# Optimization experiments

Measured on AMD Instinct MI355X. Metric: run time of the kernel, lower is better.

## Reference

```python
import jax, jax.numpy as jnp
import numpy as np

IN_F = 2048
OUT_F = 8192
NUM_BLOCKS = 2097152  # (IN_F*OUT_F)//8
K = 4096
BLOCK = 8

def setup_inputs() -> dict:
    key = jax.random.key(0)
    k1, k2, k3, k4 = jax.random.split(key, 4)
    x = jax.random.normal(k1, (4, 2048, IN_F), dtype=jnp.float32)
    codebook = jax.random.normal(k2, (K, BLOCK), dtype=jnp.float32)
    indices = jax.random.randint(k3, (NUM_BLOCKS,), 0, K, dtype=jnp.int64)
    bias = jax.random.normal(k4, (OUT_F,), dtype=jnp.float32)
    return {"x": x, "codebook": codebook, "indices": indices, "bias": bias}

def reference(x, codebook, indices, bias):
    # Dequantize: gather codewords and reassemble the full weight matrix.
    # codebook[indices]: (num_blocks, block) -> flatten -> (in_f, out_f)
    W = codebook[indices].reshape(IN_F, OUT_F)
    # GPT-2 Conv1D: out = x @ W + b  (W is (in, out), not transposed)
    out = jnp.matmul(x, W) + bias
    return out
```

## Files before the change

### kernel.cpp

```cpp
#include <hip/hip_runtime.h>
#include <hip/hip_bf16.h>

typedef unsigned short ushort_t;
typedef __attribute__((ext_vector_type(8))) short short8;
typedef __attribute__((ext_vector_type(4))) float f32x4;

#define M_DIM 8192
#define N_DIM 8192
#define K_DIM 2048
#define BM 256
#define BN 256
#define BK 64
#define NT (K_DIM / BK)

__device__ __forceinline__ ushort_t f2bf(float f) {
    union { float f; unsigned u; } v; v.f = f;
    unsigned r = v.u + 0x7fffu + ((v.u >> 16) & 1u);
    return (ushort_t)(r >> 16);
}

__device__ __forceinline__ void async_copy16(const void* g, void* l) {
    __builtin_amdgcn_global_load_lds(
        (const __attribute__((address_space(1))) void*)g,
        (__attribute__((address_space(3))) void*)l, 16, 0, 0);
}

#define BAR() __builtin_amdgcn_s_barrier()
#define LGKM0() do { asm volatile("s_waitcnt lgkmcnt(0)" ::: "memory"); \
                     __builtin_amdgcn_sched_barrier(0); } while (0)

__global__ __launch_bounds__(256) void convert_x(const float* __restrict__ x,
                                                 ushort_t* __restrict__ A) {
    int t = blockIdx.x * 256 + threadIdx.x;
    const float4* p = (const float4*)x + (size_t)t * 2;
    float4 a = p[0], b = p[1];
    short8 o;
    o[0] = (short)f2bf(a.x); o[1] = (short)f2bf(a.y);
    o[2] = (short)f2bf(a.z); o[3] = (short)f2bf(a.w);
    o[4] = (short)f2bf(b.x); o[5] = (short)f2bf(b.y);
    o[6] = (short)f2bf(b.z); o[7] = (short)f2bf(b.w);
    *(short8*)(A + (size_t)t * 8) = o;
}

__global__ __launch_bounds__(256) void dequant_wt(const int* __restrict__ indices,
                                                  const float* __restrict__ codebook,
                                                  ushort_t* __restrict__ Bt) {
    int g = blockIdx.x;
    int i = blockIdx.y * 256 + threadIdx.x;
    int idx = indices[(size_t)i * 1024 + g];
    const float4* cb = (const float4*)(codebook + (size_t)idx * 8);
    float4 lo = cb[0], hi = cb[1];
    size_t base = (size_t)g * 8 * K_DIM + i;
    Bt[base + 0 * K_DIM] = f2bf(lo.x);
    Bt[base + 1 * K_DIM] = f2bf(lo.y);
    Bt[base + 2 * K_DIM] = f2bf(lo.z);
    Bt[base + 3 * K_DIM] = f2bf(lo.w);
    Bt[base + 4 * K_DIM] = f2bf(hi.x);
    Bt[base + 5 * K_DIM] = f2bf(hi.y);
    Bt[base + 6 * K_DIM] = f2bf(hi.z);
    Bt[base + 7 * K_DIM] = f2bf(hi.w);
}

__device__ __forceinline__ void load_af4(const ushort_t* p, const int (&off)[4][2],
                                         short8 (&fr)[4][2]) {
#pragma unroll
    for (int i = 0; i < 4; ++i)
#pragma unroll
        for (int kk = 0; kk < 2; ++kk)
            fr[i][kk] = *(const short8*)((const char*)p + off[i][kk]);
}

__device__ __forceinline__ void load_bf2(const ushort_t* p, const int (&off)[2][2],
                                         short8 (&fr)[2][2]) {
#pragma unroll
    for (int j = 0; j < 2; ++j)
#pragma unroll
        for (int kk = 0; kk < 2; ++kk)
            fr[j][kk] = *(const short8*)((const char*)p + off[j][kk]);
}

__device__ __forceinline__ void mfma16(const short8 (&af)[4][2], const short8 (&bf)[2][2],
                                       f32x4 (&acc)[8][4], int I0, int J0) {
    __builtin_amdgcn_s_setprio(1);
#pragma unroll
    for (int kk = 0; kk < 2; ++kk)
#pragma unroll
        for (int i = 0; i < 4; ++i)
#pragma unroll
            for (int j = 0; j < 2; ++j)
                acc[I0 + i][J0 + j] = __builtin_amdgcn_mfma_f32_16x16x32_bf16(
                    af[i][kk], bf[j][kk], acc[I0 + i][J0 + j], 0, 0, 0);
    __builtin_amdgcn_s_setprio(0);
}

__global__ __launch_bounds__(512, 2) void gemm_256_8phase(const ushort_t* __restrict__ A,
                                                          const ushort_t* __restrict__ Bt,
                                                          const float* __restrict__ bias,
                                                          float* __restrict__ C) {
    __shared__ __align__(16) ushort_t lds_a[2][2][128 * 64];
    __shared__ __align__(16) ushort_t lds_b[2][2][128 * 64];

    const int bid = blockIdx.x;
    const int x = bid & 7;
    const int q = bid >> 3;
    const int mt = ((x >> 1) << 2) + (q & 3) + (((q >> 5) & 1) << 4);
    const int nt = ((x & 1) << 3) + ((q >> 2) & 7) + (((q >> 6) & 1) << 4);
    const int m0 = mt * BM;
    const int n0 = nt * BN;

    const int tid = threadIdx.x;
    const int lane = tid & 63;
    const int wid = tid >> 6;
    const int wm = wid >> 2, wn = wid & 3;
    const int lane15 = lane & 15, laneq = lane >> 4;

    const int G0 = tid, G1 = 512 + tid;
    const int r0 = G0 >> 3, r1 = G1 >> 3;
    const int c0 = (G0 & 7) ^ (r0 & 7), c1 = (G1 & 7) ^ (r1 & 7);
    const size_t aoff0 = (size_t)(m0 + r0) * K_DIM + c0 * 8;
    const size_t aoff1 = (size_t)(m0 + r1) * K_DIM + c1 * 8;
    const size_t boff0 = (size_t)(n0 + r0) * K_DIM + c0 * 8;
    const size_t boff1 = (size_t)(n0 + r1) * K_DIM + c1 * 8;
    const int dq0 = G0 * 16, dq1 = G1 * 16;
    const size_t HOFF = (size_t)128 * K_DIM;

#define STAGE_A(gt, hh) do { \
        char* _d = (char*)&lds_a[(gt) & 1][hh][0]; \
        async_copy16(A + aoff0 + (size_t)(hh) * HOFF + (size_t)(gt) * BK, _d + dq0); \
        async_copy16(A + aoff1 + (size_t)(hh) * HOFF + (size_t)(gt) * BK, _d + dq1); \
    } while (0)
#define STAGE_B(gt, hh) do { \
        char* _d = (char*)&lds_b[(gt) & 1][hh][0]; \
        async_copy16(Bt + boff0 + (size_t)(hh) * HOFF + (size_t)(gt) * BK, _d + dq0); \
        async_copy16(Bt + boff1 + (size_t)(hh) * HOFF + (size_t)(gt) * BK, _d + dq1); \
    } while (0)

    int offA[4][2], offB[2][2];
#pragma unroll
    for (int i = 0; i < 4; ++i) {
        int row = wm * 64 + i * 16 + lane15;
#pragma unroll
        for (int kk = 0; kk < 2; ++kk)
            offA[i][kk] = row * 128 + (((kk * 4 + laneq) ^ (row & 7)) * 16);
    }
#pragma unroll
    for (int j = 0; j < 2; ++j) {
        int row = wn * 32 + j * 16 + lane15;
#pragma unroll
        for (int kk = 0; kk < 2; ++kk)
            offB[j][kk] = row * 128 + (((kk * 4 + laneq) ^ (row & 7)) * 16);
    }

    f32x4 acc[8][4];
#pragma unroll
    for (int i = 0; i < 8; ++i)
#pragma unroll
        for (int j = 0; j < 4; ++j) acc[i][j] = (f32x4){0.f, 0.f, 0.f, 0.f};

    STAGE_A(0, 0); STAGE_B(0, 0); STAGE_B(0, 1); STAGE_A(0, 1);
    STAGE_B(1, 0); STAGE_B(1, 1); STAGE_A(1, 1);
    asm volatile("s_waitcnt vmcnt(6)" ::: "memory");
    BAR();

    short8 af[4][2], bf0[2][2], bf1[2][2];

    for (int g = 0; g < NT; ++g) {
        const int d = g & 1;
        load_af4(&lds_a[d][0][0], offA, af);
        load_bf2(&lds_b[d][0][0], offB, bf0);
        if (g + 1 < NT) STAGE_A(g + 1, 0);
        asm volatile("s_waitcnt lgkmcnt(8)" ::: "memory");
        BAR(); LGKM0();
        mfma16(af, bf0, acc, 0, 0);
        BAR();
        load_bf2(&lds_b[d][1][0], offB, bf1);
        if (g + 2 < NT) STAGE_B(g + 2, 0);
        BAR(); LGKM0();
        mfma16(af, bf1, acc, 0, 2);
        BAR();
        load_af4(&lds_a[d][1][0], offA, af);
        if (g + 2 < NT) STAGE_B(g + 2, 1);
        BAR(); LGKM0();
        mfma16(af, bf1, acc, 4, 2);
        BAR();
        if (g + 2 < NT) STAGE_A(g + 2, 1);
        BAR(); LGKM0();
        mfma16(af, bf0, acc, 4, 0);
        if (g < NT - 2) { asm volatile("s_waitcnt vmcnt(6)" ::: "memory"); }
        else            { asm volatile("s_waitcnt vmcnt(0)" ::: "memory"); }
        BAR();
    }

#pragma unroll
    for (int ig = 0; ig < 8; ++ig) {
        int row = m0 + (ig >> 2) * 128 + wm * 64 + (ig & 3) * 16 + laneq * 4;
#pragma unroll
        for (int jg = 0; jg < 4; ++jg) {
            int col = n0 + (jg >> 1) * 128 + wn * 32 + (jg & 1) * 16 + lane15;
            float bv = bias[col];
            f32x4 v = acc[ig][jg];
#pragma unroll
            for (int q2 = 0; q2 < 4; ++q2)
                C[(size_t)(row + q2) * N_DIM + col] = v[q2] + bv;
        }
    }
#undef STAGE_A
#undef STAGE_B
}

extern "C" void kernel_launch(void* const* d_in, const int* in_sizes, int n_in,
                              void* d_out, int out_size, void* d_ws, size_t ws_size,
                              hipStream_t stream) {
    const float* x = (const float*)d_in[0];
    const float* codebook = (const float*)d_in[1];
    const int* indices = (const int*)d_in[2];
    const float* bias = (const float*)d_in[3];
    float* out = (float*)d_out;

    ushort_t* A  = (ushort_t*)d_ws;
    ushort_t* Bt = (ushort_t*)d_ws + (size_t)M_DIM * K_DIM;

    convert_x<<<dim3(M_DIM * K_DIM / (256 * 8)), 256, 0, stream>>>(x, A);
    dequant_wt<<<dim3(1024, 8), 256, 0, stream>>>(indices, codebook, Bt);
    gemm_256_8phase<<<dim3((M_DIM / BM) * (N_DIM / BN)), 512, 0, stream>>>(A, Bt, bias, out);
}
```

Measured before the change: 301.9 us.

## Make GEMM persistent: each block computes four 256x256 tiles with continuous pipeline

The GEMM launch drops from 1024 blocks to 256. Each block walks a 2x2 group of 256x256 output tiles in snake order, so the async LDS prefetch pipeline runs across tile boundaries without refilling. Each finished tile is written out with bias from inside the main loop and the accumulators are reset. This removes per-block prologue and tail costs and lets the next tile's loads overlap the epilogue stores. In exchange only 256 blocks run, which may underfill the 256 CUs at 2 blocks per CU, and the inline epilogue adds register pressure.

Result: no change. 307.7 us (+1.9%).

```diff
diff --git a/kernel.cpp b/kernel.cpp
--- a/kernel.cpp
+++ b/kernel.cpp
@@ -12,6 +12,8 @@
 #define BN 256
 #define BK 64
 #define NT (K_DIM / BK)
+#define TT 4
+#define GTOT (TT * NT)
 
 __device__ __forceinline__ ushort_t f2bf(float f) {
     union { float f; unsigned u; } v; v.f = f;
@@ -93,6 +95,9 @@
     __builtin_amdgcn_s_setprio(0);
 }
 
+__device__ __forceinline__ int tile_tm(int t) { return t >> 1; }
+__device__ __forceinline__ int tile_tn(int t) { return (t & 1) ^ (t >> 1); }
+
 __global__ __launch_bounds__(512, 2) void gemm_256_8phase(const ushort_t* __restrict__ A,
                                                           const ushort_t* __restrict__ Bt,
                                                           const float* __restrict__ bias,
@@ -102,11 +107,11 @@
 
     const int bid = blockIdx.x;
     const int x = bid & 7;
-    const int q = bid >> 3;
-    const int mt = ((x >> 1) << 2) + (q & 3) + (((q >> 5) & 1) << 4);
-    const int nt = ((x & 1) << 3) + ((q >> 2) & 7) + (((q >> 6) & 1) << 4);
-    const int m0 = mt * BM;
-    const int n0 = nt * BN;
+    const int u = bid >> 3;
+    const int st_m = (x >> 1) * 4 + (u & 3);
+    const int st_n = (x & 1) * 8 + ((u >> 2) & 7);
+    const int m_base = st_m * 512;
+    const int n_base = st_n * 512;
 
     const int tid = threadIdx.x;
     const int lane = tid & 63;
@@ -117,22 +122,26 @@
     const int G0 = tid, G1 = 512 + tid;
     const int r0 = G0 >> 3, r1 = G1 >> 3;
     const int c0 = (G0 & 7) ^ (r0 & 7), c1 = (G1 & 7) ^ (r1 & 7);
-    const size_t aoff0 = (size_t)(m0 + r0) * K_DIM + c0 * 8;
-    const size_t aoff1 = (size_t)(m0 + r1) * K_DIM + c1 * 8;
-    const size_t boff0 = (size_t)(n0 + r0) * K_DIM + c0 * 8;
-    const size_t boff1 = (size_t)(n0 + r1) * K_DIM + c1 * 8;
+    const size_t aoff0 = (size_t)(m_base + r0) * K_DIM + c0 * 8;
+    const size_t aoff1 = (size_t)(m_base + r1) * K_DIM + c1 * 8;
+    const size_t boff0 = (size_t)(n_base + r0) * K_DIM + c0 * 8;
+    const size_t boff1 = (size_t)(n_base + r1) * K_DIM + c1 * 8;
     const int dq0 = G0 * 16, dq1 = G1 * 16;
     const size_t HOFF = (size_t)128 * K_DIM;
 
-#define STAGE_A(gt, hh) do { \
-        char* _d = (char*)&lds_a[(gt) & 1][hh][0]; \
-        async_copy16(A + aoff0 + (size_t)(hh) * HOFF + (size_t)(gt) * BK, _d + dq0); \
-        async_copy16(A + aoff1 + (size_t)(hh) * HOFF + (size_t)(gt) * BK, _d + dq1); \
+#define STAGE_A(h, hh) do { \
+        int _t = (h) >> 5, _k = (h) & 31; \
+        size_t _mo = (size_t)(tile_tm(_t) * 256) * K_DIM; \
+        char* _d = (char*)&lds_a[(h) & 1][hh][0]; \
+        async_copy16(A + aoff0 + _mo + (size_t)(hh) * HOFF + (size_t)_k * BK, _d + dq0); \
+        async_copy16(A + aoff1 + _mo + (size_t)(hh) * HOFF + (size_t)_k * BK, _d + dq1); \
     } while (0)
-#define STAGE_B(gt, hh) do { \
-        char* _d = (char*)&lds_b[(gt) & 1][hh][0]; \
-        async_copy16(Bt + boff0 + (size_t)(hh) * HOFF + (size_t)(gt) * BK, _d + dq0); \
-        async_copy16(Bt + boff1 + (size_t)(hh) * HOFF + (size_t)(gt) * BK, _d + dq1); \
+#define STAGE_B(h, hh) do { \
+        int _t = (h) >> 5, _k = (h) & 31; \
+        size_t _no = (size_t)(tile_tn(_t) * 256) * K_DIM; \
+        char* _d = (char*)&lds_b[(h) & 1][hh][0]; \
+        async_copy16(Bt + boff0 + _no + (size_t)(hh) * HOFF + (size_t)_k * BK, _d + dq0); \
+        async_copy16(Bt + boff1 + _no + (size_t)(hh) * HOFF + (size_t)_k * BK, _d + dq1); \
     } while (0)
 
     int offA[4][2], offB[2][2];
@@ -164,44 +173,53 @@
 
     short8 af[4][2], bf0[2][2], bf1[2][2];
 
-    for (int g = 0; g < NT; ++g) {
+    for (int g = 0; g < GTOT; ++g) {
         const int d = g & 1;
         load_af4(&lds_a[d][0][0], offA, af);
         load_bf2(&lds_b[d][0][0], offB, bf0);
-        if (g + 1 < NT) STAGE_A(g + 1, 0);
+        if (g + 1 < GTOT) STAGE_A(g + 1, 0);
         asm volatile("s_waitcnt lgkmcnt(8)" ::: "memory");
         BAR(); LGKM0();
         mfma16(af, bf0, acc, 0, 0);
         BAR();
         load_bf2(&lds_b[d][1][0], offB, bf1);
-        if (g + 2 < NT) STAGE_B(g + 2, 0);
+        if (g + 2 < GTOT) STAGE_B(g + 2, 0);
         BAR(); LGKM0();
         mfma16(af, bf1, acc, 0, 2);
         BAR();
         load_af4(&lds_a[d][1][0], offA, af);
-        if (g + 2 < NT) STAGE_B(g + 2, 1);
+        if (g + 2 < GTOT) STAGE_B(g + 2, 1);
         BAR(); LGKM0();
         mfma16(af, bf1, acc, 4, 2);
         BAR();
-        if (g + 2 < NT) STAGE_A(g + 2, 1);
+        if (g + 2 < GTOT) STAGE_A(g + 2, 1);
         BAR(); LGKM0();
         mfma16(af, bf0, acc, 4, 0);
-        if (g < NT - 2) { asm volatile("s_waitcnt vmcnt(6)" ::: "memory"); }
-        else            { asm volatile("s_waitcnt vmcnt(0)" ::: "memory"); }
-        BAR();
-    }
-
-#pragma unroll
-    for (int ig = 0; ig < 8; ++ig) {
-        int row = m0 + (ig >> 2) * 128 + wm * 64 + (ig & 3) * 16 + laneq * 4;
-#pragma unroll
-        for (int jg = 0; jg < 4; ++jg) {
-            int col = n0 + (jg >> 1) * 128 + wn * 32 + (jg & 1) * 16 + lane15;
-            float bv = bias[col];
-            f32x4 v = acc[ig][jg];
-#pragma unroll
-            for (int q2 = 0; q2 < 4; ++q2)
-                C[(size_t)(row + q2) * N_DIM + col] = v[q2] + bv;
+        if (g < GTOT - 2) { asm volatile("s_waitcnt vmcnt(6)" ::: "memory"); }
+        else              { asm volatile("s_waitcnt vmcnt(0)" ::: "memory"); }
+        BAR();
+
+        if ((g & 31) == 31) {
+            const int t = g >> 5;
+            const int tm0 = m_base + tile_tm(t) * 256;
+            const int tn0 = n_base + tile_tn(t) * 256;
+#pragma unroll
+            for (int ig = 0; ig < 8; ++ig) {
+                int row = tm0 + (ig >> 2) * 128 + wm * 64 + (ig & 3) * 16 + laneq * 4;
+#pragma unroll
+                for (int jg = 0; jg < 4; ++jg) {
+                    int col = tn0 + (jg >> 1) * 128 + wn * 32 + (jg & 1) * 16 + lane15;
+                    float bv = bias[col];
+                    f32x4 v = acc[ig][jg];
+#pragma unroll
+                    for (int q2 = 0; q2 < 4; ++q2)
+                        C[(size_t)(row + q2) * N_DIM + col] = v[q2] + bv;
+                }
+            }
+#pragma unroll
+            for (int i = 0; i < 8; ++i)
+#pragma unroll
+                for (int j = 0; j < 4; ++j) acc[i][j] = (f32x4){0.f, 0.f, 0.f, 0.f};
         }
     }
 #undef STAGE_A
@@ -222,5 +240,5 @@
 
     convert_x<<<dim3(M_DIM * K_DIM / (256 * 8)), 256, 0, stream>>>(x, A);
     dequant_wt<<<dim3(1024, 8), 256, 0, stream>>>(indices, codebook, Bt);
-    gemm_256_8phase<<<dim3((M_DIM / BM) * (N_DIM / BN)), 512, 0, stream>>>(A, Bt, bias, out);
-}
+    gemm_256_8phase<<<dim3(256), 512, 0, stream>>>(A, Bt, bias, out);
+}
```
